# Kernel tuning notes

Measured on AMD Instinct MI355X. Metric: run time of the kernel, lower is better.

Reference implementation:

```python
import jax, jax.numpy as jnp
import numpy as np

B, N, F = 2, 2048, 1024
H, E = 512, 256   # feature_sizes = [1024, 512, 256]
K = 30            # K_max


def setup_inputs() -> dict:
    key = jax.random.key(0)
    k0, k1, k2, k3, k4 = jax.random.split(key, 5)
    x = jax.random.normal(k0, (B, N, F), dtype=jnp.float32)
    s0 = 1.0 / np.sqrt(F)
    s1 = 1.0 / np.sqrt(H)
    # torch.nn.Linear default init: U(-1/sqrt(fan_in), 1/sqrt(fan_in)), weight [out, in]
    W0 = jax.random.uniform(k1, (H, F), jnp.float32, -s0, s0)
    b0 = jax.random.uniform(k2, (H,), jnp.float32, -s0, s0)
    W1 = jax.random.uniform(k3, (E, H), jnp.float32, -s1, s1)
    b1 = jax.random.uniform(k4, (E,), jnp.float32, -s1, s1)
    return {"x": x, "W0": W0, "b0": b0, "W1": W1, "b1": b1}


def _osg_single(xs, W0, b0, W1, b1):
    # xs: [N, F] (no NaNs, so masked_select(~isnan) is identity)
    # DIST (EMBEDDING + cosine)
    h = jax.nn.relu(xs @ W0.T + b0)          # [N, H]
    e = h @ W1.T + b1                         # [N, E]
    corr = e @ e.T                            # [N, N]
    d = jnp.diagonal(corr)                    # [N]
    denom = jnp.sqrt(jnp.clip(d[:, None] * d[None, :], 1e-8, None))
    D = (1.0 - corr / denom) / 2.0            # [N, N]

    # D_SUM_CALC: D_sum[i, j] (j >= i) = sum of D[i:j+1, i:j+1] (block sums)
    # via padded 2D prefix sums. Only the upper triangle is consumed downstream.
    Sp = jnp.pad(jnp.cumsum(jnp.cumsum(D, axis=0), axis=1), ((1, 0), (1, 0)))  # [N+1, N+1]
    dS = jnp.diagonal(Sp)                     # [N+1]
    Bsum = dS[1:][None, :] - Sp[:-1, 1:] - Sp[1:, :-1].T + dS[:-1][:, None]    # [N, N]

    idx = jnp.arange(N)
    BIG = jnp.float32(1e30)
    C0 = Bsum[:, N - 1]                       # C[n, 0] = D_sum[n, N-1]

    # C_TABLE_ALL DP over k, fused with the per-column masked mean:
    # T_pred[i] = mean over all C_all[nn, kk, i] >= 0.
    # k = 0 layer: C_all[n, 0, N-1] = 1 for every n (N entries in column N-1).
    tsum0 = jnp.zeros((N,), jnp.float32).at[N - 1].set(float(N))
    tcnt0 = jnp.zeros((N,), jnp.float32).at[N - 1].set(float(N))

    def step(carry, kk):
        Cprev, tsum, tcnt = carry
        # Cshift[i] = C[i+1, kk-1]; pad value never used (i+1 <= N-kk <= N-1)
        Cshift = jnp.concatenate([Cprev[1:], jnp.zeros((1,), Cprev.dtype)])
        M = Bsum + Cshift[None, :]            # M[nn, i] = D_sum[nn, i] + C[i+1, kk-1]
        valid = (idx[None, :] >= idx[:, None]) & (idx[None, :] < N - kk)  # i in [nn, N-kk)
        Ck = jnp.where(idx < N - kk,
                       jnp.min(jnp.where(valid, M, BIG), axis=1),
                       0.0)                    # torch leaves C at 0 for invalid rows
        soft = jax.nn.softmax(jnp.where(valid, -M, -BIG), axis=1)  # Softmin over valid i
        tsum = tsum + jnp.sum(jnp.where(valid, soft, 0.0), axis=0)
        tcnt = tcnt + jnp.sum(valid, axis=0).astype(tsum.dtype)
        return (Ck, tsum, tcnt), None

    (_, tsum, tcnt), _ = jax.lax.scan(step, (C0, tsum0, tcnt0), jnp.arange(1, K))
    return tsum / tcnt                        # every column has count >= 1 for K >= 2


def reference(x, W0, b0, W1, b1):
    # N == x.shape[1] (no NaN padding needed), so T_out is [B, N]
    return jax.vmap(lambda xs: _osg_single(xs, W0, b0, W1, b1))(x)
```

## Files before the change

### kernel.cpp

```cpp
#include <hip/hip_runtime.h>
#include <hip/hip_bf16.h>
#include <float.h>

#define NTOK 2048
#define FDIM 1024
#define HDIM 512
#define EDIM 256
#define BATCH 2
#define KSEG 30
#define NP1 2049
static const size_t ST2 = (size_t)NP1 * NP1;

template<int MODE>
__global__ __launch_bounds__(256)
void gemm_nt(const float* __restrict__ A, int lda,
             const float* __restrict__ Bm, int ldb,
             const float* __restrict__ bias,
             float* __restrict__ C, int ldc, int K)
{
    __shared__ float As[32][68];
    __shared__ float Bs[32][68];
    const float* Ab = A;
    const float* Bb = Bm;

    const int t = threadIdx.x;
    const int tx = t & 15, ty = t >> 4;
    const int lrow = t >> 3, lkv = t & 7;
    const int by = blockIdx.y, bx = blockIdx.x;

    float acc[4][4] = {};
    const int ktiles = K >> 5;
    for (int kt = 0; kt < ktiles; ++kt) {
#pragma unroll
        for (int h = 0; h < 2; ++h) {
            const int r = lrow + h * 32;
            const float4 av = *(const float4*)(Ab + (size_t)(by * 64 + r) * lda + kt * 32 + lkv * 4);
            As[lkv * 4 + 0][r] = av.x; As[lkv * 4 + 1][r] = av.y;
            As[lkv * 4 + 2][r] = av.z; As[lkv * 4 + 3][r] = av.w;
            const float4 bv = *(const float4*)(Bb + (size_t)(bx * 64 + r) * ldb + kt * 32 + lkv * 4);
            Bs[lkv * 4 + 0][r] = bv.x; Bs[lkv * 4 + 1][r] = bv.y;
            Bs[lkv * 4 + 2][r] = bv.z; Bs[lkv * 4 + 3][r] = bv.w;
        }
        __syncthreads();
#pragma unroll
        for (int kk = 0; kk < 32; ++kk) {
            const float4 a = *(const float4*)&As[kk][ty * 4];
            const float4 b = *(const float4*)&Bs[kk][tx * 4];
            const float ar[4] = {a.x, a.y, a.z, a.w};
            const float br[4] = {b.x, b.y, b.z, b.w};
#pragma unroll
            for (int i = 0; i < 4; ++i)
#pragma unroll
                for (int j = 0; j < 4; ++j)
                    acc[i][j] = fmaf(ar[i], br[j], acc[i][j]);
        }
        __syncthreads();
    }

    const int row0 = by * 64 + ty * 4;
    const int col0 = bx * 64 + tx * 4;
#pragma unroll
    for (int i = 0; i < 4; ++i) {
        float o[4];
#pragma unroll
        for (int j = 0; j < 4; ++j) {
            float v = acc[i][j] + bias[col0 + j];
            if (MODE == 0) v = fmaxf(v, 0.0f);
            o[j] = v;
        }
        float4 v4; v4.x = o[0]; v4.y = o[1]; v4.z = o[2]; v4.w = o[3];
        *(float4*)(C + (size_t)(row0 + i) * ldc + col0) = v4;
    }
}

__global__ __launch_bounds__(256)
void gemm_corr(const float* __restrict__ E, float* __restrict__ D,
               const float* __restrict__ dvec)
{
    __shared__ float As[16][140];
    __shared__ float Bs[16][140];
    const int z = blockIdx.z;
    const float* Eb = E + (size_t)z * NTOK * EDIM;
    float* Db = D + (size_t)z * NTOK * NTOK;
    const int t = threadIdx.x;
    const int tx = t & 15, ty = t >> 4;
    const int by = blockIdx.y, bx = blockIdx.x;
    const int fq = t & 3, lr = t >> 2;

    float acc[8][8] = {};
    for (int kt = 0; kt < EDIM / 16; ++kt) {
#pragma unroll
        for (int h = 0; h < 2; ++h) {
            const int r = lr + h * 64;
            const int rr = r + 4 * (r >> 5);
            const float4 av = *(const float4*)(Eb + (size_t)(by * 128 + r) * EDIM + kt * 16 + fq * 4);
            As[fq * 4 + 0][rr] = av.x; As[fq * 4 + 1][rr] = av.y;
            As[fq * 4 + 2][rr] = av.z; As[fq * 4 + 3][rr] = av.w;
            const float4 bv = *(const float4*)(Eb + (size_t)(bx * 128 + r) * EDIM + kt * 16 + fq * 4);
            Bs[fq * 4 + 0][rr] = bv.x; Bs[fq * 4 + 1][rr] = bv.y;
            Bs[fq * 4 + 2][rr] = bv.z; Bs[fq * 4 + 3][rr] = bv.w;
        }
        __syncthreads();
        const int ma = 8 * ty + 4 * (ty >> 2);
        const int mb = 8 * tx + 4 * (tx >> 2);
#pragma unroll
        for (int k = 0; k < 16; ++k) {
            const float4 a0 = *(const float4*)&As[k][ma];
            const float4 a1 = *(const float4*)&As[k][ma + 4];
            const float4 b0 = *(const float4*)&Bs[k][mb];
            const float4 b1 = *(const float4*)&Bs[k][mb + 4];
            const float ar[8] = {a0.x, a0.y, a0.z, a0.w, a1.x, a1.y, a1.z, a1.w};
            const float br[8] = {b0.x, b0.y, b0.z, b0.w, b1.x, b1.y, b1.z, b1.w};
#pragma unroll
            for (int i = 0; i < 8; ++i)
#pragma unroll
                for (int j = 0; j < 8; ++j)
                    acc[i][j] = fmaf(ar[i], br[j], acc[i][j]);
        }
        __syncthreads();
    }

    const int row0 = by * 128 + ty * 8;
    const int col0 = bx * 128 + tx * 8;
    float di[8], dj[8];
#pragma unroll
    for (int i = 0; i < 8; ++i) di[i] = dvec[z * NTOK + row0 + i];
#pragma unroll
    for (int j = 0; j < 8; ++j) dj[j] = dvec[z * NTOK + col0 + j];
#pragma unroll
    for (int i = 0; i < 8; ++i) {
        float o[8];
#pragma unroll
        for (int j = 0; j < 8; ++j) {
            const float den = sqrtf(fmaxf(di[i] * dj[j], 1e-8f));
            o[j] = 0.5f * (1.0f - acc[i][j] / den);
        }
        float4 w0; w0.x = o[0]; w0.y = o[1]; w0.z = o[2]; w0.w = o[3];
        float4 w1; w1.x = o[4]; w1.y = o[5]; w1.z = o[6]; w1.w = o[7];
        *(float4*)(Db + (size_t)(row0 + i) * NTOK + col0) = w0;
        *(float4*)(Db + (size_t)(row0 + i) * NTOK + col0 + 4) = w1;
    }
}

__global__ __launch_bounds__(256)
void rownorm_kernel(const float* __restrict__ e, float* __restrict__ dvec)
{
    const int wid = (blockIdx.x * 256 + threadIdx.x) >> 6;
    const int lane = threadIdx.x & 63;
    if (wid >= BATCH * NTOK) return;
    const float4 v = *(const float4*)(e + (size_t)wid * EDIM + lane * 4);
    float s = v.x * v.x + v.y * v.y + v.z * v.z + v.w * v.w;
#pragma unroll
    for (int off = 32; off; off >>= 1) s += __shfl_xor(s, off);
    if (lane == 0) dvec[wid] = s;
}

__global__ __launch_bounds__(256)
void sat_row_kernel(const float* __restrict__ D, double* __restrict__ Sp)
{
    const int b = blockIdx.y;
    const int r = blockIdx.x + 1;
    const float* drow = D + (size_t)b * NTOK * NTOK + (size_t)(r - 1) * NTOK;
    double* sprow = Sp + (size_t)b * ST2 + (size_t)r * NP1;
    const int t = threadIdx.x, lane = t & 63, wv = t >> 6;
    __shared__ double wtot[4];
    double carry = 0.0;
    if (t == 0) sprow[0] = 0.0;
    for (int ch = 0; ch < NTOK / 256; ++ch) {
        double v = (double)drow[ch * 256 + t];
#pragma unroll
        for (int d = 1; d < 64; d <<= 1) {
            const double u = __shfl_up(v, (unsigned)d, 64);
            if (lane >= d) v += u;
        }
        if (lane == 63) wtot[wv] = v;
        __syncthreads();
        double pre = carry;
        for (int ww = 0; ww < wv; ++ww) pre += wtot[ww];
        const double tot = carry + wtot[0] + wtot[1] + wtot[2] + wtot[3];
        sprow[ch * 256 + t + 1] = v + pre;
        __syncthreads();
        carry = tot;
    }
}

__global__ void satc1(const double* __restrict__ Sp, double* __restrict__ aux)
{
    const int b = blockIdx.z, s = blockIdx.y;
    const int c = blockIdx.x * 256 + threadIdx.x;
    if (c > NTOK) return;
    const double* sp = Sp + (size_t)b * ST2;
    double tt = 0.0;
    const int r0 = s * 256 + 1;
    for (int r = r0; r < r0 + 256; ++r) tt += sp[(size_t)r * NP1 + c];
    aux[(size_t)(b * 8 + s) * NP1 + c] = tt;
}
__global__ void satc2(double* __restrict__ aux)
{
    const int b = blockIdx.y;
    const int c = blockIdx.x * 256 + threadIdx.x;
    if (c > NTOK) return;
    double run = 0.0;
    for (int s = 0; s < 8; ++s) {
        const size_t id = (size_t)(b * 8 + s) * NP1 + c;
        const double tt = aux[id]; aux[id] = run; run += tt;
    }
}
__global__ void satc3(double* __restrict__ Sp, const double* __restrict__ aux)
{
    const int b = blockIdx.z, s = blockIdx.y;
    const int c = blockIdx.x * 256 + threadIdx.x;
    if (c > NTOK) return;
    double* sp = Sp + (size_t)b * ST2;
    if (s == 0) sp[c] = 0.0;
    double run = aux[(size_t)(b * 8 + s) * NP1 + c];
    const int r0 = s * 256 + 1;
    for (int r = r0; r < r0 + 256; ++r) {
        const size_t id = (size_t)r * NP1 + c;
        run += sp[id];
        sp[id] = run;
    }
}

__global__ void diag_kernel(const double* __restrict__ Sp, double* __restrict__ dg)
{
    const int b = blockIdx.y;
    const int t = blockIdx.x * 256 + threadIdx.x;
    if (t <= NTOK) dg[b * NP1 + t] = Sp[(size_t)b * ST2 + (size_t)t * NP1 + t];
}

__global__ __launch_bounds__(256)
void bsum_kernel(const double* __restrict__ Sp, const double* __restrict__ dg,
                 float* __restrict__ Bsum, float* __restrict__ C0)
{
    const int b = blockIdx.y, i = blockIdx.x;
    const double* sprow = Sp + (size_t)b * ST2 + (size_t)i * NP1;
    const double* dgb = dg + (size_t)b * NP1;
    const double di = dgb[i];
    float* brow = Bsum + (size_t)b * NTOK * NTOK + (size_t)i * NTOK;
    for (int j = i + threadIdx.x; j < NTOK; j += 256) {
        const double v = dgb[j + 1] + di - 2.0 * sprow[j + 1];
        brow[j] = (float)v;
        if (j == NTOK - 1) C0[b * NTOK + i] = (float)v;
    }
}

#define DP_BX 128
#define DP_PAIRS 8
#define RBBIG 3.0e37f

__device__ inline void cstore(float* p, float v)
{
    __hip_atomic_store(p, v, __ATOMIC_RELAXED, __HIP_MEMORY_SCOPE_AGENT);
}

__device__ inline void wait_flags(const int* flagsb, int need)
{
    if (threadIdx.x < DP_BX) {
        const int* f = flagsb + threadIdx.x * 4;
        while (__hip_atomic_load(f, __ATOMIC_RELAXED, __HIP_MEMORY_SCOPE_AGENT) < need)
            __builtin_amdgcn_s_sleep(1);
    }
    __syncthreads();
}

__device__ inline void publish(int* myflag, int val)
{
    asm volatile("s_waitcnt vmcnt(0)" ::: "memory");
    __syncthreads();
    if (threadIdx.x == 0)
        __hip_atomic_store(myflag, val, __ATOMIC_RELAXED, __HIP_MEMORY_SCOPE_AGENT);
}

template<int NC>
__device__ inline void load_rb(const float* __restrict__ brow, int colbase, int lane,
                               float (&rb)[NC])
{
#pragma unroll
    for (int c = 0; c < NC; ++c) {
        const int col = colbase + lane + c * 64;
        rb[c] = (col < NTOK) ? brow[col] : RBBIG;
    }
}

template<int NC>
__device__ inline float pass1(const float (&rb)[NC], const float* __restrict__ cs,
                              int coff, int V, int lane)
{
    float mn = FLT_MAX;
#pragma unroll
    for (int c = 0; c < NC; ++c) {
        const int idx = lane + c * 64;
        if (idx < V) mn = fminf(mn, rb[c] + cs[coff + idx]);
    }
#pragma unroll
    for (int o = 32; o; o >>= 1) mn = fminf(mn, __shfl_xor(mn, o));
    return mn;
}

template<int NC>
__device__ inline void pass2(const float (&rb)[NC], const float* __restrict__ cs,
                             int coff, int V, float mn, int lane, float (&ac)[NC])
{
    float w[NC];
    float s = 0.0f;
#pragma unroll
    for (int c = 0; c < NC; ++c) {
        const int idx = lane + c * 64;
        float x = 0.0f;
        if (idx < V) x = __expf(mn - (rb[c] + cs[coff + idx]));
        w[c] = x;
        s += x;
    }
#pragma unroll
    for (int o = 32; o; o >>= 1) s += __shfl_xor(s, o);
    const float inv = 1.0f / s;
#pragma unroll
    for (int c = 0; c < NC; ++c) ac[c] = __builtin_fmaf(w[c], inv, ac[c]);
}

template<int NC>
__device__ inline void merge_acc(const float (&ac)[NC], int base, int lane,
                                 float* __restrict__ acc_lds)
{
#pragma unroll
    for (int c = 0; c < NC; ++c) {
        const int col = base + lane + c * 64;
        if (col < NTOK && ac[c] != 0.0f) atomicAdd(&acc_lds[col], ac[c]);
    }
}

__global__ __launch_bounds__(256, 1)
void dp_fused_kernel(const float* __restrict__ Bsum,
                     float* __restrict__ Ca, float* __restrict__ Cb,
                     float* __restrict__ tsum, int* __restrict__ flags)
{
    __shared__ float cs[NTOK];
    __shared__ float acc_lds[NTOK];
    const int b = blockIdx.y;
    const int t = threadIdx.x, lane = t & 63, wv = t >> 6;
    const float* Bb = Bsum + (size_t)b * NTOK * NTOK;
    const int pbase = blockIdx.x * DP_PAIRS;
    int* flagsb = flags + b * DP_BX * 4;
    int* myflag = flagsb + blockIdx.x * 4;

    const int p0 = pbase + wv * 2, p1 = p0 + 1;
    const int i1_0 = NTOK - 1 - p0, i1_1 = NTOK - 1 - p1;

    float rbA0[32], rbB0[16], rbA1[32], rbB1[16];
    load_rb<32>(Bb + (size_t)p0 * NTOK, p0, lane, rbA0);
    load_rb<16>(Bb + (size_t)i1_0 * NTOK, i1_0, lane, rbB0);
    load_rb<32>(Bb + (size_t)p1 * NTOK, p1, lane, rbA1);
    load_rb<16>(Bb + (size_t)i1_1 * NTOK, i1_1, lane, rbB1);

    float acA0[32] = {}, acB0[16] = {}, acA1[32] = {}, acB1[16] = {};

    for (int j = t; j < NTOK; j += 256) acc_lds[j] = 0.0f;

    if (t < DP_PAIRS) {
        const int p = pbase + t, i1 = NTOK - 1 - p;
        if (p > 0) cstore(&Ca[b * NTOK + p - 1], Bb[(size_t)p * NTOK + NTOK - 1]);
        cstore(&Ca[b * NTOK + i1 - 1], Bb[(size_t)i1 * NTOK + NTOK - 1]);
    }
    publish(myflag, 0);

    const float* Cr = Ca;
    float* Cn = Cb;

    for (int k = 1; k < KSEG; ++k) {
        wait_flags(flagsb, k - 1);
        {
            const unsigned long long* Cr8 = (const unsigned long long*)(Cr + b * NTOK);
            unsigned long long* cs8 = (unsigned long long*)cs;
#pragma unroll
            for (int r = 0; r < NTOK / 2 / 256; ++r)
                cs8[t + r * 256] = __hip_atomic_load(&Cr8[t + r * 256],
                                                     __ATOMIC_RELAXED, __HIP_MEMORY_SCOPE_AGENT);
        }
        __syncthreads();
        float* Cnb = Cn + b * NTOK;
        const int jmax = NTOK - k;

        const int VA0 = jmax - p0, VA1 = jmax - p1;
        const int VB0 = p0 + 1 - k, VB1 = p1 + 1 - k;
        const float mnA0 = pass1<32>(rbA0, cs, p0, VA0, lane);
        float mnB0 = 0.0f, mnB1 = 0.0f;
        if (p0 >= k) mnB0 = pass1<16>(rbB0, cs, i1_0, VB0, lane);
        const float mnA1 = pass1<32>(rbA1, cs, p1, VA1, lane);
        if (p1 >= k) mnB1 = pass1<16>(rbB1, cs, i1_1, VB1, lane);
        if (lane == 0) {
            if (p0 > 0) cstore(&Cnb[p0 - 1], mnA0);
            cstore(&Cnb[i1_0 - 1], (p0 >= k) ? mnB0 : 0.0f);
            cstore(&Cnb[p1 - 1], mnA1);
            cstore(&Cnb[i1_1 - 1], (p1 >= k) ? mnB1 : 0.0f);
        }
        publish(myflag, k);

        pass2<32>(rbA0, cs, p0, VA0, mnA0, lane, acA0);
        if (p0 >= k) pass2<16>(rbB0, cs, i1_0, VB0, mnB0, lane, acB0);
        pass2<32>(rbA1, cs, p1, VA1, mnA1, lane, acA1);
        if (p1 >= k) pass2<16>(rbB1, cs, i1_1, VB1, mnB1, lane, acB1);

        float* tmp = (float*)Cr; Cr = Cn; Cn = tmp;
    }

    __syncthreads();
    merge_acc<32>(acA0, p0, lane, acc_lds);
    merge_acc<16>(acB0, i1_0, lane, acc_lds);
    merge_acc<32>(acA1, p1, lane, acc_lds);
    merge_acc<16>(acB1, i1_1, lane, acc_lds);
    __syncthreads();
    float* ts = tsum + b * NTOK;
    for (int j = t; j < NTOK; j += 256) {
        const float v = acc_lds[j];
        if (v != 0.0f) atomicAdd(&ts[j], v);
    }
}

__global__ __launch_bounds__(256)
void dp_step_kernel(const float* __restrict__ Bsum, const float* __restrict__ Cprev,
                    float* __restrict__ Cnext, float* __restrict__ tsum, int kk)
{
    __shared__ float cs[NTOK];
    __shared__ float acc[NTOK];
    const int b = blockIdx.y;
    const int t = threadIdx.x, lane = t & 63, wv = t >> 6;
    const float* Cp = Cprev + b * NTOK;
    for (int j = t; j < NTOK; j += 256) {
        cs[j] = (j < NTOK - 1) ? Cp[j + 1] : 0.0f;
        acc[j] = 0.0f;
    }
    __syncthreads();
    const int jmax = NTOK - kk;
    const int w = blockIdx.x * 4 + wv;
    const float* Bb = Bsum + (size_t)b * NTOK * NTOK;
    float* Cn = Cnext + b * NTOK;
    const int rows[4] = { w, 1023 - w, 1024 + w, 2047 - w };
#pragma unroll
    for (int rr = 0; rr < 4; ++rr) {
        const int i = rows[rr];
        if (i >= jmax) { if (lane == 0) Cn[i] = 0.0f; continue; }
        const float* brow = Bb + (size_t)i * NTOK;
        const int j0 = i + lane;
        float mv[32];
        float mn = FLT_MAX;
#pragma unroll
        for (int c = 0; c < 32; ++c) {
            const int j = j0 + c * 64;
            float v = FLT_MAX;
            if (j < jmax) v = brow[j] + cs[j];
            mv[c] = v;
            mn = fminf(mn, v);
        }
#pragma unroll
        for (int off = 32; off; off >>= 1) mn = fminf(mn, __shfl_xor(mn, off));
        if (lane == 0) Cn[i] = mn;
        float s = 0.0f;
#pragma unroll
        for (int c = 0; c < 32; ++c) {
            const int j = j0 + c * 64;
            float p = 0.0f;
            if (j < jmax) p = __expf(mn - mv[c]);
            mv[c] = p;
            s += p;
        }
#pragma unroll
        for (int off = 32; off; off >>= 1) s += __shfl_xor(s, off);
        const float inv = 1.0f / s;
#pragma unroll
        for (int c = 0; c < 32; ++c) {
            const int j = j0 + c * 64;
            if (j < jmax) atomicAdd(&acc[j], mv[c] * inv);
        }
    }
    __syncthreads();
    float* ts = tsum + b * NTOK;
    for (int j = t; j < NTOK; j += 256) {
        const float v = acc[j];
        if (v != 0.0f) atomicAdd(&ts[j], v);
    }
}

__global__ void finalize_kernel(const float* __restrict__ tsum, float* __restrict__ out)
{
    const int b = blockIdx.y;
    const int j = blockIdx.x * 256 + threadIdx.x;
    if (j >= NTOK) return;
    float ts = tsum[b * NTOK + j];
    int steps = NTOK - 1 - j;
    if (steps > KSEG - 1) steps = KSEG - 1;
    float tc = (float)(j + 1) * (float)steps;
    if (j == NTOK - 1) { ts += (float)NTOK; tc += (float)NTOK; }
    out[b * NTOK + j] = ts / tc;
}

extern "C" void kernel_launch(void* const* d_in, const int* in_sizes, int n_in,
                              void* d_out, int out_size, void* d_ws, size_t ws_size,
                              hipStream_t stream)
{
    const float* x  = (const float*)d_in[0];
    const float* W0 = (const float*)d_in[1];
    const float* b0 = (const float*)d_in[2];
    const float* W1 = (const float*)d_in[3];
    const float* b1 = (const float*)d_in[4];
    float* out = (float*)d_out;

    char* ws = (char*)d_ws;
    size_t off = 0;
    auto alloc = [&](size_t bytes) -> void* {
        void* p = (void*)(ws + off);
        off += (bytes + 255) & ~(size_t)255;
        return p;
    };
    double* Sp   = (double*)alloc((size_t)BATCH * ST2 * sizeof(double));
    float*  Dm   = (float*) alloc((size_t)BATCH * NTOK * NTOK * sizeof(float));
    float*  h    = (float*) alloc((size_t)BATCH * NTOK * HDIM * sizeof(float));
    float*  e    = (float*) alloc((size_t)BATCH * NTOK * EDIM * sizeof(float));
    float*  dvec = (float*) alloc((size_t)BATCH * NTOK * sizeof(float));
    double* dg   = (double*)alloc((size_t)BATCH * NP1 * sizeof(double));
    double* aux  = (double*)alloc((size_t)BATCH * 8 * NP1 * sizeof(double));
    float*  CA   = (float*) alloc((size_t)BATCH * NTOK * sizeof(float));
    float*  CB   = (float*) alloc((size_t)BATCH * NTOK * sizeof(float));
    float*  tsum = (float*) alloc((size_t)BATCH * NTOK * sizeof(float));
    int*    flags= (int*)   alloc((size_t)BATCH * DP_BX * 4 * sizeof(int));
    (void)ws_size; (void)in_sizes; (void)n_in; (void)out_size;

    hipMemsetAsync(tsum, 0, (size_t)BATCH * NTOK * sizeof(float), stream);
    hipMemsetAsync(flags, 0xFF, (size_t)BATCH * DP_BX * 4 * sizeof(int), stream);

    gemm_nt<0><<<dim3(HDIM / 64, (BATCH * NTOK) / 64), 256, 0, stream>>>(
        x, FDIM, W0, FDIM, b0, h, HDIM, FDIM);
    gemm_nt<1><<<dim3(EDIM / 64, (BATCH * NTOK) / 64), 256, 0, stream>>>(
        h, HDIM, W1, HDIM, b1, e, EDIM, HDIM);
    rownorm_kernel<<<dim3((BATCH * NTOK) / 4), 256, 0, stream>>>(e, dvec);
    gemm_corr<<<dim3(NTOK / 128, NTOK / 128, BATCH), 256, 0, stream>>>(e, Dm, dvec);
    sat_row_kernel<<<dim3(NTOK, BATCH), 256, 0, stream>>>(Dm, Sp);
    satc1<<<dim3((NP1 + 255) / 256, 8, BATCH), 256, 0, stream>>>(Sp, aux);
    satc2<<<dim3((NP1 + 255) / 256, BATCH), 256, 0, stream>>>(aux);
    satc3<<<dim3((NP1 + 255) / 256, 8, BATCH), 256, 0, stream>>>(Sp, aux);
    diag_kernel<<<dim3((NP1 + 255) / 256, BATCH), 256, 0, stream>>>(Sp, dg);
    bsum_kernel<<<dim3(NTOK, BATCH), 256, 0, stream>>>(Sp, dg, Dm, CA);

    void* args[] = { (void*)&Dm, (void*)&CA, (void*)&CB, (void*)&tsum, (void*)&flags };
    hipError_t err = hipLaunchCooperativeKernel((const void*)dp_fused_kernel,
                                                dim3(DP_BX, BATCH), dim3(256),
                                                args, 0, stream);
    if (err != hipSuccess) {
        float* cp = CA; float* cn = CB;
        for (int kk = 1; kk < KSEG; ++kk) {
            dp_step_kernel<<<dim3(128, BATCH), 256, 0, stream>>>(Dm, cp, cn, tsum, kk);
            float* tmp = cp; cp = cn; cn = tmp;
        }
    }
    finalize_kernel<<<dim3(NTOK / 256, BATCH), 256, 0, stream>>>(tsum, out);
}
```

Before: 755.8 us.

## Use 128x128 split-K GEMM for first layer and inline-asm DP state loads

```diff
diff --git a/kernel.cpp b/kernel.cpp
--- a/kernel.cpp
+++ b/kernel.cpp
@@ -11,18 +11,14 @@
 #define NP1 2049
 static const size_t ST2 = (size_t)NP1 * NP1;
 
-template<int MODE>
-__global__ __launch_bounds__(256)
-void gemm_nt(const float* __restrict__ A, int lda,
-             const float* __restrict__ Bm, int ldb,
-             const float* __restrict__ bias,
-             float* __restrict__ C, int ldc, int K)
+__global__ __launch_bounds__(256)
+void gemm_nt64(const float* __restrict__ A, int lda,
+               const float* __restrict__ Bm, int ldb,
+               const float* __restrict__ bias,
+               float* __restrict__ C, int ldc, int K)
 {
     __shared__ float As[32][68];
     __shared__ float Bs[32][68];
-    const float* Ab = A;
-    const float* Bb = Bm;
-
     const int t = threadIdx.x;
     const int tx = t & 15, ty = t >> 4;
     const int lrow = t >> 3, lkv = t & 7;
@@ -34,10 +30,10 @@
 #pragma unroll
         for (int h = 0; h < 2; ++h) {
             const int r = lrow + h * 32;
-            const float4 av = *(const float4*)(Ab + (size_t)(by * 64 + r) * lda + kt * 32 + lkv * 4);
+            const float4 av = *(const float4*)(A + (size_t)(by * 64 + r) * lda + kt * 32 + lkv * 4);
             As[lkv * 4 + 0][r] = av.x; As[lkv * 4 + 1][r] = av.y;
             As[lkv * 4 + 2][r] = av.z; As[lkv * 4 + 3][r] = av.w;
-            const float4 bv = *(const float4*)(Bb + (size_t)(bx * 64 + r) * ldb + kt * 32 + lkv * 4);
+            const float4 bv = *(const float4*)(Bm + (size_t)(bx * 64 + r) * ldb + kt * 32 + lkv * 4);
             Bs[lkv * 4 + 0][r] = bv.x; Bs[lkv * 4 + 1][r] = bv.y;
             Bs[lkv * 4 + 2][r] = bv.z; Bs[lkv * 4 + 3][r] = bv.w;
         }
@@ -61,16 +57,87 @@
     const int col0 = bx * 64 + tx * 4;
 #pragma unroll
     for (int i = 0; i < 4; ++i) {
-        float o[4];
-#pragma unroll
-        for (int j = 0; j < 4; ++j) {
-            float v = acc[i][j] + bias[col0 + j];
-            if (MODE == 0) v = fmaxf(v, 0.0f);
-            o[j] = v;
-        }
-        float4 v4; v4.x = o[0]; v4.y = o[1]; v4.z = o[2]; v4.w = o[3];
+        float4 v4;
+        v4.x = acc[i][0] + bias[col0 + 0];
+        v4.y = acc[i][1] + bias[col0 + 1];
+        v4.z = acc[i][2] + bias[col0 + 2];
+        v4.w = acc[i][3] + bias[col0 + 3];
         *(float4*)(C + (size_t)(row0 + i) * ldc + col0) = v4;
     }
+}
+
+__global__ __launch_bounds__(256)
+void gemm_nt128s(const float* __restrict__ A, int lda,
+                 const float* __restrict__ Bm, int ldb,
+                 float* __restrict__ Cp, int ldc, int M, int khalf)
+{
+    __shared__ float As[16][140];
+    __shared__ float Bs[16][140];
+    const int t = threadIdx.x;
+    const int tx = t & 15, ty = t >> 4;
+    const int by = blockIdx.y, bx = blockIdx.x;
+    const int k0 = blockIdx.z * khalf;
+    const int fq = t & 3, lr = t >> 2;
+
+    float acc[8][8] = {};
+    for (int kt = 0; kt < khalf / 16; ++kt) {
+#pragma unroll
+        for (int h = 0; h < 2; ++h) {
+            const int r = lr + h * 64;
+            const int rr = r + 4 * (r >> 5);
+            const float4 av = *(const float4*)(A + (size_t)(by * 128 + r) * lda + k0 + kt * 16 + fq * 4);
+            As[fq * 4 + 0][rr] = av.x; As[fq * 4 + 1][rr] = av.y;
+            As[fq * 4 + 2][rr] = av.z; As[fq * 4 + 3][rr] = av.w;
+            const float4 bv = *(const float4*)(Bm + (size_t)(bx * 128 + r) * ldb + k0 + kt * 16 + fq * 4);
+            Bs[fq * 4 + 0][rr] = bv.x; Bs[fq * 4 + 1][rr] = bv.y;
+            Bs[fq * 4 + 2][rr] = bv.z; Bs[fq * 4 + 3][rr] = bv.w;
+        }
+        __syncthreads();
+        const int ma = 8 * ty + 4 * (ty >> 2);
+        const int mb = 8 * tx + 4 * (tx >> 2);
+#pragma unroll
+        for (int k = 0; k < 16; ++k) {
+            const float4 a0 = *(const float4*)&As[k][ma];
+            const float4 a1 = *(const float4*)&As[k][ma + 4];
+            const float4 b0 = *(const float4*)&Bs[k][mb];
+            const float4 b1 = *(const float4*)&Bs[k][mb + 4];
+            const float ar[8] = {a0.x, a0.y, a0.z, a0.w, a1.x, a1.y, a1.z, a1.w};
+            const float br[8] = {b0.x, b0.y, b0.z, b0.w, b1.x, b1.y, b1.z, b1.w};
+#pragma unroll
+            for (int i = 0; i < 8; ++i)
+#pragma unroll
+                for (int j = 0; j < 8; ++j)
+                    acc[i][j] = fmaf(ar[i], br[j], acc[i][j]);
+        }
+        __syncthreads();
+    }
+
+    float* outp = Cp + (size_t)blockIdx.z * M * ldc;
+    const int row0 = by * 128 + ty * 8;
+    const int col0 = bx * 128 + tx * 8;
+#pragma unroll
+    for (int i = 0; i < 8; ++i) {
+        float4 w0; w0.x = acc[i][0]; w0.y = acc[i][1]; w0.z = acc[i][2]; w0.w = acc[i][3];
+        float4 w1; w1.x = acc[i][4]; w1.y = acc[i][5]; w1.z = acc[i][6]; w1.w = acc[i][7];
+        *(float4*)(outp + (size_t)(row0 + i) * ldc + col0) = w0;
+        *(float4*)(outp + (size_t)(row0 + i) * ldc + col0 + 4) = w1;
+    }
+}
+
+__global__ __launch_bounds__(256)
+void combine_relu(const float* __restrict__ p0, const float* __restrict__ p1,
+                  const float* __restrict__ bias, float* __restrict__ hout)
+{
+    const int idx = blockIdx.x * 256 + threadIdx.x;
+    const float4 a = ((const float4*)p0)[idx];
+    const float4 b = ((const float4*)p1)[idx];
+    const float4 bs = *(const float4*)&bias[(idx & 127) * 4];
+    float4 o;
+    o.x = fmaxf(a.x + b.x + bs.x, 0.0f);
+    o.y = fmaxf(a.y + b.y + bs.y, 0.0f);
+    o.z = fmaxf(a.z + b.z + bs.z, 0.0f);
+    o.w = fmaxf(a.w + b.w + bs.w, 0.0f);
+    ((float4*)hout)[idx] = o;
 }
 
 __global__ __launch_bounds__(256)
@@ -370,12 +437,18 @@
     for (int k = 1; k < KSEG; ++k) {
         wait_flags(flagsb, k - 1);
         {
-            const unsigned long long* Cr8 = (const unsigned long long*)(Cr + b * NTOK);
-            unsigned long long* cs8 = (unsigned long long*)cs;
-#pragma unroll
-            for (int r = 0; r < NTOK / 2 / 256; ++r)
-                cs8[t + r * 256] = __hip_atomic_load(&Cr8[t + r * 256],
-                                                     __ATOMIC_RELAXED, __HIP_MEMORY_SCOPE_AGENT);
+            const float* base  = Cr + b * NTOK + t * 4;
+            const float* base2 = base + 1024;
+            float4 va, vb;
+            asm volatile(
+                "global_load_dwordx4 %0, %2, off sc1\n\t"
+                "global_load_dwordx4 %1, %3, off sc1\n\t"
+                "s_waitcnt vmcnt(0)"
+                : "=&v"(va), "=&v"(vb)
+                : "v"(base), "v"(base2)
+                : "memory");
+            *(float4*)&cs[t * 4] = va;
+            *(float4*)&cs[t * 4 + 1024] = vb;
         }
         __syncthreads();
         float* Cnb = Cn + b * NTOK;
@@ -528,9 +601,12 @@
     hipMemsetAsync(tsum, 0, (size_t)BATCH * NTOK * sizeof(float), stream);
     hipMemsetAsync(flags, 0xFF, (size_t)BATCH * DP_BX * 4 * sizeof(int), stream);
 
-    gemm_nt<0><<<dim3(HDIM / 64, (BATCH * NTOK) / 64), 256, 0, stream>>>(
-        x, FDIM, W0, FDIM, b0, h, HDIM, FDIM);
-    gemm_nt<1><<<dim3(EDIM / 64, (BATCH * NTOK) / 64), 256, 0, stream>>>(
+    float* Hpart = Dm;
+    gemm_nt128s<<<dim3(HDIM / 128, (BATCH * NTOK) / 128, 2), 256, 0, stream>>>(
+        x, FDIM, W0, FDIM, Hpart, HDIM, BATCH * NTOK, FDIM / 2);
+    combine_relu<<<dim3((BATCH * NTOK * HDIM / 4) / 256), 256, 0, stream>>>(
+        Hpart, Hpart + (size_t)BATCH * NTOK * HDIM, b0, h);
+    gemm_nt64<<<dim3(EDIM / 64, (BATCH * NTOK) / 64), 256, 0, stream>>>(
         h, HDIM, W1, HDIM, b1, e, EDIM, HDIM);
     rownorm_kernel<<<dim3((BATCH * NTOK) / 4), 256, 0, stream>>>(e, dvec);
     gemm_corr<<<dim3(NTOK / 128, NTOK / 128, BATCH), 256, 0, stream>>>(e, Dm, dvec);
```

After: 739.4 us. -2.2%, faster.
